# Performance work log

Measured on AMD Instinct MI355X. Metric: run time of the kernel, lower is better.

The kernel has to match this reference:

```python
import jax, jax.numpy as jnp
import numpy as np

N_NODES = 100000
N_EDGES = 1600000
IN_DIM = 64
HID_DIM = 64
OUT_DIM = 1


def setup_inputs() -> dict:
    key = jax.random.key(0)
    ks = jax.random.split(key, 5)
    x = jax.random.normal(ks[0], (N_NODES, IN_DIM), dtype=jnp.float32)
    edge_index = jax.random.randint(ks[1], (2, N_EDGES), 0, N_NODES, dtype=jnp.int64)
    s1 = 1.0 / np.sqrt(IN_DIM)
    s2 = 1.0 / np.sqrt(HID_DIM)
    W1 = jax.random.normal(ks[2], (IN_DIM, HID_DIM), dtype=jnp.float32) * s1
    b1 = jnp.zeros((HID_DIM,), dtype=jnp.float32)
    W2 = jax.random.normal(ks[3], (HID_DIM, HID_DIM), dtype=jnp.float32) * s2
    b2 = jnp.zeros((HID_DIM,), dtype=jnp.float32)
    Wp = jax.random.normal(ks[4], (HID_DIM, OUT_DIM), dtype=jnp.float32) * s2
    bp = jnp.zeros((OUT_DIM,), dtype=jnp.float32)
    return {"x": x, "edge_index": edge_index, "W1": W1, "b1": b1,
            "W2": W2, "b2": b2, "Wp": Wp, "bp": bp}


def _gcn_conv(x, src, dst, deg_inv_sqrt, W, b):
    # PyG GCNConv: linear transform, then deg-normalized scatter-add aggregation
    h = x @ W  # [N, out]
    norm = deg_inv_sqrt[src] * deg_inv_sqrt[dst]  # [E_total]
    msg = h[src] * norm[:, None]  # gather + scale, [E_total, out]
    agg = jax.ops.segment_sum(msg, dst, num_segments=x.shape[0])
    return agg + b


def reference(x, edge_index, W1, b1, W2, b2, Wp, bp):
    n = x.shape[0]
    # add self-loops (as PyG GCNConv does by default)
    loop = jnp.arange(n, dtype=edge_index.dtype)
    src = jnp.concatenate([edge_index[0], loop])
    dst = jnp.concatenate([edge_index[1], loop])
    # symmetric normalization from in-degree over dst (includes self-loops)
    deg = jax.ops.segment_sum(jnp.ones_like(dst, dtype=x.dtype), dst, num_segments=n)
    deg_inv_sqrt = jnp.where(deg > 0, jax.lax.rsqrt(jnp.maximum(deg, 1e-12)), 0.0)
    h = jax.nn.relu(_gcn_conv(x, src, dst, deg_inv_sqrt, W1, b1))
    # dropout(p=0.3) is identity at eval time
    h = jax.nn.relu(_gcn_conv(h, src, dst, deg_inv_sqrt, W2, b2))
    return h @ Wp + bp  # [N, OUT_DIM]
```

## Files before the change

### kernel.cpp

```cpp
#include <hip/hip_runtime.h>
#include <hip/hip_fp16.h>


#define GNN_N 100000
#define GNN_E 1600000
#define NBUCK 391
#define NBLK  250
#define EPB   6400
#define SCTILE 16
#define STAGE_CAP 4864
#define DUMMY_OFF (GNN_N * 128)

__global__ __launch_bounds__(256) void k_hist(const int* __restrict__ dst,
                                              int* __restrict__ hist,
                                              __half* __restrict__ TA,
                                              __half* __restrict__ TB) {
    __shared__ int h[NBUCK];
    for (int i = threadIdx.x; i < NBUCK; i += 256) h[i] = 0;
    if (blockIdx.x == 0 && threadIdx.x < 16) {
        uint4 z = {0, 0, 0, 0};
        int t = threadIdx.x;
        __half* base = (t < 8) ? TA : TB;
        *(uint4*)((char*)base + DUMMY_OFF + (t & 7) * 16) = z;
    }
    __syncthreads();
    int b = blockIdx.x;
    int e0 = b * EPB, e1 = min(e0 + EPB, GNN_E);
    for (int e = e0 + threadIdx.x * 4; e < e1; e += 1024) {
        int4 d = *(const int4*)(dst + e);
        atomicAdd(&h[d.x >> 8], 1);
        atomicAdd(&h[d.y >> 8], 1);
        atomicAdd(&h[d.z >> 8], 1);
        atomicAdd(&h[d.w >> 8], 1);
    }
    __syncthreads();
    for (int i = threadIdx.x; i < NBUCK; i += 256)
        hist[b * NBUCK + i] = h[i];
}

__global__ __launch_bounds__(256) void k_cscan(int* __restrict__ hist,
                                               int* __restrict__ tot) {
    __shared__ int tile[256][SCTILE + 1];
    int k0 = blockIdx.x * SCTILE;
    int b = threadIdx.x;
#pragma unroll
    for (int i = 0; i < SCTILE; ++i) {
        int k = k0 + i;
        tile[b][i] = (k < NBUCK && b < NBLK) ? hist[b * NBUCK + k] : 0;
    }
    __syncthreads();
    int lane = b & 63, w = b >> 6;
    int cSub = lane >> 4;
    int l16 = lane & 15;
    int col = w * 4 + cSub;
    int run = 0;
    for (int chunk = 0; chunk < 16; ++chunk) {
        int idx = chunk * 16 + l16;
        int v = tile[idx][col];
        int s = v;
#pragma unroll
        for (int o = 1; o < 16; o <<= 1) {
            int t = __shfl_up(s, o);
            if (l16 >= o) s += t;
        }
        tile[idx][col] = s - v + run;
        run += __shfl(s, lane | 15);
    }
    if (l16 == 0 && k0 + col < NBUCK) tot[k0 + col] = run;
    __syncthreads();
#pragma unroll
    for (int i = 0; i < SCTILE; ++i) {
        int k = k0 + i;
        if (k < NBUCK && b < NBLK) hist[b * NBUCK + k] = tile[b][i];
    }
}

__global__ __launch_bounds__(512) void k_btot(const int* __restrict__ tot,
                                              int* __restrict__ bbase,
                                              int* __restrict__ cbase) {
    __shared__ int s[NBUCK];
    int t = threadIdx.x;
    if (t < NBUCK) s[t] = tot[t];
    __syncthreads();
    if (t == 0) {
        int run = 0;
        for (int i = 0; i < NBUCK; ++i) { int v = s[i]; s[i] = run; run += v; }
    }
    __syncthreads();
    if (t < NBUCK) {
        bbase[t] = s[t];
        cbase[t] = (s[t] & ~3) + t * 772;
    }
    if (t == 0) bbase[NBUCK] = GNN_E;
}

__global__ __launch_bounds__(256) void k_part(const int* __restrict__ src,
                                              const int* __restrict__ dst,
                                              const int* __restrict__ hist,
                                              const int* __restrict__ bbase,
                                              unsigned int* __restrict__ part) {
    __shared__ int off[NBUCK];
    int b = blockIdx.x;
    for (int i = threadIdx.x; i < NBUCK; i += 256)
        off[i] = bbase[i] + hist[b * NBUCK + i];
    __syncthreads();
    int e0 = b * EPB, e1 = min(e0 + EPB, GNN_E);
    for (int e = e0 + threadIdx.x * 4; e < e1; e += 1024) {
        int4 d = *(const int4*)(dst + e);
        int4 s = *(const int4*)(src + e);
        int sl0 = atomicAdd(&off[d.x >> 8], 1);
        part[sl0] = ((unsigned int)(d.x & 255) << 17) | (unsigned int)s.x;
        int sl1 = atomicAdd(&off[d.y >> 8], 1);
        part[sl1] = ((unsigned int)(d.y & 255) << 17) | (unsigned int)s.y;
        int sl2 = atomicAdd(&off[d.z >> 8], 1);
        part[sl2] = ((unsigned int)(d.z & 255) << 17) | (unsigned int)s.z;
        int sl3 = atomicAdd(&off[d.w >> 8], 1);
        part[sl3] = ((unsigned int)(d.w & 255) << 17) | (unsigned int)s.w;
    }
}

__global__ __launch_bounds__(256) void k_bsort(const unsigned int* __restrict__ part,
                                               const int* __restrict__ bbase,
                                               const int* __restrict__ cbase,
                                               int* __restrict__ csr,
                                               int* __restrict__ rowptr,
                                               int* __restrict__ deg,
                                               float* __restrict__ dis) {
    __shared__ int cnt[256];
    __shared__ int pstart[256];
    __shared__ int bump[256];
    __shared__ unsigned int stage[STAGE_CAP];
    int k = blockIdx.x;
    int t = threadIdx.x;
    cnt[t] = 0;
    __syncthreads();
    int e0 = bbase[k], e1 = bbase[k + 1];
    int m = e1 - e0;
    bool fits = (m <= STAGE_CAP);
    for (int i = t; i < m; i += 256) {
        unsigned int p = part[e0 + i];
        if (fits) stage[i] = p;
        atomicAdd(&cnt[p >> 17], 1);
    }
    __syncthreads();
    if (t == 0) {
        int run = 0;
        for (int i = 0; i < 256; ++i) {
            pstart[i] = run;
            run += (cnt[i] + 3) & ~3;
        }
    }
    __syncthreads();
    int cb = cbase[k];
    int node = k * 256 + t;
    if (node < GNN_N) {
        int c = cnt[t];
        rowptr[node] = cb + pstart[t];
        deg[node]    = (c + 3) & ~3;
        dis[node]    = rsqrtf((float)c + 1.0f);
    }
    bump[t] = pstart[t];
    __syncthreads();
    for (int i = t; i < m; i += 256) {
        unsigned int p = fits ? stage[i] : part[e0 + i];
        int slot = atomicAdd(&bump[p >> 17], 1);
        csr[cb + slot] = (int)(p & 0x1FFFF) << 7;
    }
    __syncthreads();
    if (node < GNN_N) {
        int c = cnt[t], pc = (c + 3) & ~3;
        for (int i = c; i < pc; ++i)
            csr[cb + pstart[t] + i] = DUMMY_OFF;
    }
}

template<typename TIN>
__global__ __launch_bounds__(256) void k_mm64h(const TIN* __restrict__ X,
                                               const float* __restrict__ W,
                                               const float* __restrict__ dis,
                                               __half* __restrict__ Y, int n) {
    __shared__ float  Xs[64][68];
    __shared__ float4 Wsh[64 * 16];
    int tid = threadIdx.x;
    int base = blockIdx.x * 64;
    for (int i = tid; i < 1024; i += 256)
        Wsh[i] = ((const float4*)W)[i];
    if constexpr (sizeof(TIN) == 4) {
#pragma unroll
        for (int i = 0; i < 4; ++i) {
            int g = i * 256 + tid;
            int r = g >> 4, c4 = g & 15;
            int row = base + r;
            float4 v = (row < n) ? ((const float4*)(X + (size_t)row * 64))[c4]
                                 : make_float4(0.f, 0.f, 0.f, 0.f);
            *(float4*)&Xs[r][c4 * 4] = v;
        }
    } else {
#pragma unroll
        for (int i = 0; i < 2; ++i) {
            int g = i * 256 + tid;
            int r = g >> 3, c8 = g & 7;
            int row = base + r;
            float f[8];
            if (row < n) {
                uint4 u = *(const uint4*)((const __half*)X + (size_t)row * 64 + c8 * 8);
                float2 t0 = __half22float2(*(__half2*)&u.x);
                float2 t1 = __half22float2(*(__half2*)&u.y);
                float2 t2 = __half22float2(*(__half2*)&u.z);
                float2 t3 = __half22float2(*(__half2*)&u.w);
                f[0] = t0.x; f[1] = t0.y; f[2] = t1.x; f[3] = t1.y;
                f[4] = t2.x; f[5] = t2.y; f[6] = t3.x; f[7] = t3.y;
            } else {
#pragma unroll
                for (int z = 0; z < 8; ++z) f[z] = 0.f;
            }
            *(float4*)&Xs[r][c8 * 8 + 0] = make_float4(f[0], f[1], f[2], f[3]);
            *(float4*)&Xs[r][c8 * 8 + 4] = make_float4(f[4], f[5], f[6], f[7]);
        }
    }
    __syncthreads();
    int tj = tid & 15;
    int ti = tid >> 4;
    float4 a0 = {0,0,0,0}, a1 = {0,0,0,0}, a2 = {0,0,0,0}, a3 = {0,0,0,0};
#pragma unroll 1
    for (int k4 = 0; k4 < 16; ++k4) {
        float4 x0 = *(const float4*)&Xs[ti * 4 + 0][k4 * 4];
        float4 x1 = *(const float4*)&Xs[ti * 4 + 1][k4 * 4];
        float4 x2 = *(const float4*)&Xs[ti * 4 + 2][k4 * 4];
        float4 x3 = *(const float4*)&Xs[ti * 4 + 3][k4 * 4];
        float4 w0 = Wsh[(k4 * 4 + 0) * 16 + tj];
        float4 w1 = Wsh[(k4 * 4 + 1) * 16 + tj];
        float4 w2 = Wsh[(k4 * 4 + 2) * 16 + tj];
        float4 w3 = Wsh[(k4 * 4 + 3) * 16 + tj];
#define FMA4(A, XV)                                                      \
        A.x += XV.x * w0.x + XV.y * w1.x + XV.z * w2.x + XV.w * w3.x;    \
        A.y += XV.x * w0.y + XV.y * w1.y + XV.z * w2.y + XV.w * w3.y;    \
        A.z += XV.x * w0.z + XV.y * w1.z + XV.z * w2.z + XV.w * w3.z;    \
        A.w += XV.x * w0.w + XV.y * w1.w + XV.z * w2.w + XV.w * w3.w;
        FMA4(a0, x0) FMA4(a1, x1) FMA4(a2, x2) FMA4(a3, x3)
#undef FMA4
    }
#pragma unroll
    for (int q = 0; q < 4; ++q) {
        int row = base + ti * 4 + q;
        if (row < n) {
            float d = dis[row];
            float4 a = (q == 0) ? a0 : (q == 1) ? a1 : (q == 2) ? a2 : a3;
            __half2 p0 = __floats2half2_rn(a.x * d, a.y * d);
            __half2 p1 = __floats2half2_rn(a.z * d, a.w * d);
            __half2* yp = (__half2*)(Y + (size_t)row * 64);
            yp[tj * 2 + 0] = p0;
            yp[tj * 2 + 1] = p1;
        }
    }
}

#define ACC8(A, U) {                                                     \
    float2 f_;                                                           \
    f_ = __half22float2(*(__half2*)&U.x); A[0] += f_.x; A[1] += f_.y;    \
    f_ = __half22float2(*(__half2*)&U.y); A[2] += f_.x; A[3] += f_.y;    \
    f_ = __half22float2(*(__half2*)&U.z); A[4] += f_.x; A[5] += f_.y;    \
    f_ = __half22float2(*(__half2*)&U.w); A[6] += f_.x; A[7] += f_.y; }

template<bool HEAD>
__global__ __launch_bounds__(256) void k_gatherg(
        const __half* __restrict__ T, const int* __restrict__ csr,
        const int* __restrict__ rowptr, const int* __restrict__ deg,
        const float* __restrict__ dis, const float* __restrict__ bias,
        const float* __restrict__ Wp, const float* __restrict__ bp,
        void* __restrict__ outv, int n) {
    int tid = threadIdx.x;
    int q = tid & 7;
    int node = blockIdx.x * 32 + (tid >> 3);
    if (node >= n) return;
    int base = rowptr[node];
    int cnt  = deg[node];
    float dd = dis[node];
    const char* Tq = (const char*)T + q * 16;
    float a0[8], a1[8];
#pragma unroll
    for (int i = 0; i < 8; ++i) { a0[i] = 0.f; a1[i] = 0.f; }
    int j = 0;
    for (; j + 8 <= cnt; j += 8) {
        int4 c0 = *(const int4*)(csr + base + j);
        int4 c1 = *(const int4*)(csr + base + j + 4);
        uint4 u0 = *(const uint4*)(Tq + (size_t)(unsigned)c0.x);
        uint4 u1 = *(const uint4*)(Tq + (size_t)(unsigned)c0.y);
        uint4 u2 = *(const uint4*)(Tq + (size_t)(unsigned)c0.z);
        uint4 u3 = *(const uint4*)(Tq + (size_t)(unsigned)c0.w);
        uint4 u4 = *(const uint4*)(Tq + (size_t)(unsigned)c1.x);
        uint4 u5 = *(const uint4*)(Tq + (size_t)(unsigned)c1.y);
        uint4 u6 = *(const uint4*)(Tq + (size_t)(unsigned)c1.z);
        uint4 u7 = *(const uint4*)(Tq + (size_t)(unsigned)c1.w);
        ACC8(a0, u0) ACC8(a1, u1) ACC8(a0, u2) ACC8(a1, u3)
        ACC8(a0, u4) ACC8(a1, u5) ACC8(a0, u6) ACC8(a1, u7)
    }
    if (j < cnt) {
        int4 c0 = *(const int4*)(csr + base + j);
        uint4 u0 = *(const uint4*)(Tq + (size_t)(unsigned)c0.x);
        uint4 u1 = *(const uint4*)(Tq + (size_t)(unsigned)c0.y);
        uint4 u2 = *(const uint4*)(Tq + (size_t)(unsigned)c0.z);
        uint4 u3 = *(const uint4*)(Tq + (size_t)(unsigned)c0.w);
        ACC8(a0, u0) ACC8(a1, u1) ACC8(a0, u2) ACC8(a1, u3)
    }
    uint4 us = *(const uint4*)(Tq + (size_t)node * 128);
    ACC8(a1, us)
    float4 bb0 = ((const float4*)bias)[q * 2 + 0];
    float4 bb1 = ((const float4*)bias)[q * 2 + 1];
    float r[8];
    r[0] = fmaxf(dd * (a0[0] + a1[0]) + bb0.x, 0.f);
    r[1] = fmaxf(dd * (a0[1] + a1[1]) + bb0.y, 0.f);
    r[2] = fmaxf(dd * (a0[2] + a1[2]) + bb0.z, 0.f);
    r[3] = fmaxf(dd * (a0[3] + a1[3]) + bb0.w, 0.f);
    r[4] = fmaxf(dd * (a0[4] + a1[4]) + bb1.x, 0.f);
    r[5] = fmaxf(dd * (a0[5] + a1[5]) + bb1.y, 0.f);
    r[6] = fmaxf(dd * (a0[6] + a1[6]) + bb1.z, 0.f);
    r[7] = fmaxf(dd * (a0[7] + a1[7]) + bb1.w, 0.f);
    if constexpr (HEAD) {
        float4 w0 = ((const float4*)Wp)[q * 2 + 0];
        float4 w1 = ((const float4*)Wp)[q * 2 + 1];
        float s = r[0] * w0.x + r[1] * w0.y + r[2] * w0.z + r[3] * w0.w
                + r[4] * w1.x + r[5] * w1.y + r[6] * w1.z + r[7] * w1.w;
#pragma unroll
        for (int m = 1; m <= 4; m <<= 1) s += __shfl_xor(s, m);
        if (q == 0) ((float*)outv)[node] = s + bp[0];
    } else {
        __half* op = (__half*)outv + (size_t)node * 64 + q * 8;
        __half2 h0 = __floats2half2_rn(r[0], r[1]);
        __half2 h1 = __floats2half2_rn(r[2], r[3]);
        __half2 h2 = __floats2half2_rn(r[4], r[5]);
        __half2 h3 = __floats2half2_rn(r[6], r[7]);
        uint4 u;
        *(__half2*)&u.x = h0; *(__half2*)&u.y = h1;
        *(__half2*)&u.z = h2; *(__half2*)&u.w = h3;
        *(uint4*)op = u;
    }
}

extern "C" void kernel_launch(void* const* d_in, const int* in_sizes, int n_in,
                              void* d_out, int out_size, void* d_ws, size_t ws_size,
                              hipStream_t stream) {
    const float* x  = (const float*)d_in[0];
    const int*   ei = (const int*)d_in[1];
    const float* W1 = (const float*)d_in[2];
    const float* b1 = (const float*)d_in[3];
    const float* W2 = (const float*)d_in[4];
    const float* b2 = (const float*)d_in[5];
    const float* Wp = (const float*)d_in[6];
    const float* bp = (const float*)d_in[7];
    float* out = (float*)d_out;

    const int N = GNN_N, E = GNN_E;
    const int* srcv = ei;
    const int* dstv = ei + E;

    char* ws = (char*)d_ws;
    int*    hist   = (int*)(ws + 0);
    int*    bbase  = (int*)(ws + 392000);
    int*    cbase  = (int*)(ws + 393600);
    int*    rowptr = (int*)(ws + 395264);
    int*    deg    = (int*)(ws + 795264);
    float*  dis    = (float*)(ws + 1195264);
    int*    tot    = (int*)(ws + 1195264);
    int*    csr    = (int*)(ws + 1595392);
    __half* TA     = (__half*)(ws + 9600000);
    __half* h1h    = (__half*)(ws + 22400256);
    __half* TB     = (__half*)(ws + 35200384);
    unsigned int* part = (unsigned int*)(ws + 48000512);

    k_hist <<<NBLK, 256, 0, stream>>>(dstv, hist, TA, TB);
    k_cscan<<<(NBUCK + SCTILE - 1) / SCTILE, 256, 0, stream>>>(hist, tot);
    k_btot <<<1, 512, 0, stream>>>(tot, bbase, cbase);
    k_part <<<NBLK, 256, 0, stream>>>(srcv, dstv, hist, bbase, part);
    k_bsort<<<NBUCK, 256, 0, stream>>>(part, bbase, cbase, csr, rowptr, deg, dis);

    k_mm64h<float><<<(N + 63) / 64, 256, 0, stream>>>(x, W1, dis, TA, N);
    k_gatherg<false><<<(N + 31) / 32, 256, 0, stream>>>(TA, csr, rowptr, deg, dis,
                                                        b1, nullptr, nullptr, h1h, N);
    k_mm64h<__half><<<(N + 63) / 64, 256, 0, stream>>>(h1h, W2, dis, TB, N);
    k_gatherg<true><<<(N + 31) / 32, 256, 0, stream>>>(TB, csr, rowptr, deg, dis,
                                                       b2, Wp, bp, out, N);
}
```

Measured before the change: 147.7 us.

## Use MFMA for node transforms, parallelize scans, split histogram blocks

Replaces the FP32 FMA-based 64x64 node transform with fp16 MFMA 16x16x32 instructions, staging X and a transposed fp16 W in shared memory and writing the output through LDS for coalesced stores. Replaces the serial single-thread scans in k_btot and k_bsort with Hillis-Steele and wave-shuffle parallel scans. Doubles the number of histogram blocks, with k_cscan scanning in two passes and k_part reading the offset of every other sub-block. Inputs and weights are now rounded to fp16 before the matmul, which lowers precision, and k_part depends on its block aligning with an even histogram block.

New measurement: 132.0 us. -10.6%, faster.

```diff
diff --git a/kernel.cpp b/kernel.cpp
--- a/kernel.cpp
+++ b/kernel.cpp
@@ -5,11 +5,16 @@
 #define GNN_N 100000
 #define GNN_E 1600000
 #define NBUCK 391
+#define HBLK  500
+#define EPBH  3200
 #define NBLK  250
 #define EPB   6400
 #define SCTILE 16
 #define STAGE_CAP 4864
 #define DUMMY_OFF (GNN_N * 128)
+
+typedef _Float16 half8 __attribute__((ext_vector_type(8)));
+typedef float f32x4 __attribute__((ext_vector_type(4)));
 
 __global__ __launch_bounds__(256) void k_hist(const int* __restrict__ dst,
                                               int* __restrict__ hist,
@@ -25,7 +30,7 @@
     }
     __syncthreads();
     int b = blockIdx.x;
-    int e0 = b * EPB, e1 = min(e0 + EPB, GNN_E);
+    int e0 = b * EPBH, e1 = min(e0 + EPBH, GNN_E);
     for (int e = e0 + threadIdx.x * 4; e < e1; e += 1024) {
         int4 d = *(const int4*)(dst + e);
         atomicAdd(&h[d.x >> 8], 1);
@@ -43,53 +48,60 @@
     __shared__ int tile[256][SCTILE + 1];
     int k0 = blockIdx.x * SCTILE;
     int b = threadIdx.x;
-#pragma unroll
-    for (int i = 0; i < SCTILE; ++i) {
-        int k = k0 + i;
-        tile[b][i] = (k < NBUCK && b < NBLK) ? hist[b * NBUCK + k] : 0;
-    }
-    __syncthreads();
     int lane = b & 63, w = b >> 6;
     int cSub = lane >> 4;
     int l16 = lane & 15;
     int col = w * 4 + cSub;
     int run = 0;
-    for (int chunk = 0; chunk < 16; ++chunk) {
-        int idx = chunk * 16 + l16;
-        int v = tile[idx][col];
-        int s = v;
-#pragma unroll
-        for (int o = 1; o < 16; o <<= 1) {
-            int t = __shfl_up(s, o);
-            if (l16 >= o) s += t;
-        }
-        tile[idx][col] = s - v + run;
-        run += __shfl(s, lane | 15);
+    for (int pass = 0; pass < 2; ++pass) {
+        int r = pass * 256 + b;
+#pragma unroll
+        for (int i = 0; i < SCTILE; ++i) {
+            int k = k0 + i;
+            tile[b][i] = (k < NBUCK && r < HBLK) ? hist[r * NBUCK + k] : 0;
+        }
+        __syncthreads();
+        for (int chunk = 0; chunk < 16; ++chunk) {
+            int idx = chunk * 16 + l16;
+            int v = tile[idx][col];
+            int s = v;
+#pragma unroll
+            for (int o = 1; o < 16; o <<= 1) {
+                int t = __shfl_up(s, o);
+                if (l16 >= o) s += t;
+            }
+            tile[idx][col] = s - v + run;
+            run += __shfl(s, lane | 15);
+        }
+        __syncthreads();
+#pragma unroll
+        for (int i = 0; i < SCTILE; ++i) {
+            int k = k0 + i;
+            if (k < NBUCK && r < HBLK) hist[r * NBUCK + k] = tile[b][i];
+        }
+        __syncthreads();
     }
     if (l16 == 0 && k0 + col < NBUCK) tot[k0 + col] = run;
-    __syncthreads();
-#pragma unroll
-    for (int i = 0; i < SCTILE; ++i) {
-        int k = k0 + i;
-        if (k < NBUCK && b < NBLK) hist[b * NBUCK + k] = tile[b][i];
-    }
 }
 
 __global__ __launch_bounds__(512) void k_btot(const int* __restrict__ tot,
                                               int* __restrict__ bbase,
                                               int* __restrict__ cbase) {
-    __shared__ int s[NBUCK];
+    __shared__ int s[512];
     int t = threadIdx.x;
-    if (t < NBUCK) s[t] = tot[t];
-    __syncthreads();
-    if (t == 0) {
-        int run = 0;
-        for (int i = 0; i < NBUCK; ++i) { int v = s[i]; s[i] = run; run += v; }
-    }
-    __syncthreads();
+    int own = (t < NBUCK) ? tot[t] : 0;
+    s[t] = own;
+    __syncthreads();
+    for (int off = 1; off < 512; off <<= 1) {
+        int v = (t >= off) ? s[t - off] : 0;
+        __syncthreads();
+        s[t] += v;
+        __syncthreads();
+    }
     if (t < NBUCK) {
-        bbase[t] = s[t];
-        cbase[t] = (s[t] & ~3) + t * 772;
+        int ex = s[t] - own;
+        bbase[t] = ex;
+        cbase[t] = (ex & ~3) + t * 772;
     }
     if (t == 0) bbase[NBUCK] = GNN_E;
 }
@@ -102,7 +114,7 @@
     __shared__ int off[NBUCK];
     int b = blockIdx.x;
     for (int i = threadIdx.x; i < NBUCK; i += 256)
-        off[i] = bbase[i] + hist[b * NBUCK + i];
+        off[i] = bbase[i] + hist[(2 * b) * NBUCK + i];
     __syncthreads();
     int e0 = b * EPB, e1 = min(e0 + EPB, GNN_E);
     for (int e = e0 + threadIdx.x * 4; e < e1; e += 1024) {
@@ -129,6 +141,7 @@
     __shared__ int cnt[256];
     __shared__ int pstart[256];
     __shared__ int bump[256];
+    __shared__ int wtot[4];
     __shared__ unsigned int stage[STAGE_CAP];
     int k = blockIdx.x;
     int t = threadIdx.x;
@@ -143,24 +156,30 @@
         atomicAdd(&cnt[p >> 17], 1);
     }
     __syncthreads();
-    if (t == 0) {
-        int run = 0;
-        for (int i = 0; i < 256; ++i) {
-            pstart[i] = run;
-            run += (cnt[i] + 3) & ~3;
-        }
-    }
+    int c = cnt[t];
+    int padded = (c + 3) & ~3;
+    int v = padded;
+#pragma unroll
+    for (int o = 1; o < 64; o <<= 1) {
+        int u = __shfl_up(v, o);
+        if ((t & 63) >= o) v += u;
+    }
+    if ((t & 63) == 63) wtot[t >> 6] = v;
+    __syncthreads();
+    int wb = 0;
+#pragma unroll
+    for (int j = 0; j < 4; ++j)
+        if (j < (t >> 6)) wb += wtot[j];
+    pstart[t] = wb + v - padded;
+    bump[t] = pstart[t];
     __syncthreads();
     int cb = cbase[k];
     int node = k * 256 + t;
     if (node < GNN_N) {
-        int c = cnt[t];
         rowptr[node] = cb + pstart[t];
-        deg[node]    = (c + 3) & ~3;
+        deg[node]    = padded;
         dis[node]    = rsqrtf((float)c + 1.0f);
     }
-    bump[t] = pstart[t];
-    __syncthreads();
     for (int i = t; i < m; i += 256) {
         unsigned int p = fits ? stage[i] : part[e0 + i];
         int slot = atomicAdd(&bump[p >> 17], 1);
@@ -168,90 +187,80 @@
     }
     __syncthreads();
     if (node < GNN_N) {
-        int c = cnt[t], pc = (c + 3) & ~3;
-        for (int i = c; i < pc; ++i)
+        for (int i = c; i < padded; ++i)
             csr[cb + pstart[t] + i] = DUMMY_OFF;
     }
 }
 
 template<typename TIN>
-__global__ __launch_bounds__(256) void k_mm64h(const TIN* __restrict__ X,
-                                               const float* __restrict__ W,
-                                               const float* __restrict__ dis,
-                                               __half* __restrict__ Y, int n) {
-    __shared__ float  Xs[64][68];
-    __shared__ float4 Wsh[64 * 16];
+__global__ __launch_bounds__(256) void k_mmf(const TIN* __restrict__ X,
+                                             const float* __restrict__ W,
+                                             const float* __restrict__ dis,
+                                             __half* __restrict__ Y, int n) {
+    __shared__ __align__(16) __half Xs[64][72];
+    __shared__ __align__(16) __half Wt[64][72];
+    __shared__ float disS[64];
     int tid = threadIdx.x;
     int base = blockIdx.x * 64;
-    for (int i = tid; i < 1024; i += 256)
-        Wsh[i] = ((const float4*)W)[i];
+    for (int i = tid; i < 4096; i += 256) {
+        int k = i >> 6, j = i & 63;
+        Wt[j][k] = __float2half(W[i]);
+    }
+    if (tid < 64) disS[tid] = (base + tid < n) ? dis[base + tid] : 0.f;
     if constexpr (sizeof(TIN) == 4) {
 #pragma unroll
-        for (int i = 0; i < 4; ++i) {
-            int g = i * 256 + tid;
-            int r = g >> 4, c4 = g & 15;
+        for (int ii = 0; ii < 4; ++ii) {
+            int i = ii * 256 + tid;
+            int r = i >> 4, c4 = i & 15;
             int row = base + r;
-            float4 v = (row < n) ? ((const float4*)(X + (size_t)row * 64))[c4]
-                                 : make_float4(0.f, 0.f, 0.f, 0.f);
-            *(float4*)&Xs[r][c4 * 4] = v;
+            float4 vv = (row < n) ? ((const float4*)(X + (size_t)row * 64))[c4]
+                                  : make_float4(0.f, 0.f, 0.f, 0.f);
+            *(__half2*)&Xs[r][c4 * 4 + 0] = __floats2half2_rn(vv.x, vv.y);
+            *(__half2*)&Xs[r][c4 * 4 + 2] = __floats2half2_rn(vv.z, vv.w);
         }
     } else {
 #pragma unroll
-        for (int i = 0; i < 2; ++i) {
-            int g = i * 256 + tid;
-            int r = g >> 3, c8 = g & 7;
+        for (int ii = 0; ii < 2; ++ii) {
+            int i = ii * 256 + tid;
+            int r = i >> 3, c8 = i & 7;
             int row = base + r;
-            float f[8];
-            if (row < n) {
-                uint4 u = *(const uint4*)((const __half*)X + (size_t)row * 64 + c8 * 8);
-                float2 t0 = __half22float2(*(__half2*)&u.x);
-                float2 t1 = __half22float2(*(__half2*)&u.y);
-                float2 t2 = __half22float2(*(__half2*)&u.z);
-                float2 t3 = __half22float2(*(__half2*)&u.w);
-                f[0] = t0.x; f[1] = t0.y; f[2] = t1.x; f[3] = t1.y;
-                f[4] = t2.x; f[5] = t2.y; f[6] = t3.x; f[7] = t3.y;
-            } else {
-#pragma unroll
-                for (int z = 0; z < 8; ++z) f[z] = 0.f;
-            }
-            *(float4*)&Xs[r][c8 * 8 + 0] = make_float4(f[0], f[1], f[2], f[3]);
-            *(float4*)&Xs[r][c8 * 8 + 4] = make_float4(f[4], f[5], f[6], f[7]);
-        }
-    }
-    __syncthreads();
-    int tj = tid & 15;
-    int ti = tid >> 4;
-    float4 a0 = {0,0,0,0}, a1 = {0,0,0,0}, a2 = {0,0,0,0}, a3 = {0,0,0,0};
-#pragma unroll 1
-    for (int k4 = 0; k4 < 16; ++k4) {
-        float4 x0 = *(const float4*)&Xs[ti * 4 + 0][k4 * 4];
-        float4 x1 = *(const float4*)&Xs[ti * 4 + 1][k4 * 4];
-        float4 x2 = *(const float4*)&Xs[ti * 4 + 2][k4 * 4];
-        float4 x3 = *(const float4*)&Xs[ti * 4 + 3][k4 * 4];
-        float4 w0 = Wsh[(k4 * 4 + 0) * 16 + tj];
-        float4 w1 = Wsh[(k4 * 4 + 1) * 16 + tj];
-        float4 w2 = Wsh[(k4 * 4 + 2) * 16 + tj];
-        float4 w3 = Wsh[(k4 * 4 + 3) * 16 + tj];
-#define FMA4(A, XV)                                                      \
-        A.x += XV.x * w0.x + XV.y * w1.x + XV.z * w2.x + XV.w * w3.x;    \
-        A.y += XV.x * w0.y + XV.y * w1.y + XV.z * w2.y + XV.w * w3.y;    \
-        A.z += XV.x * w0.z + XV.y * w1.z + XV.z * w2.z + XV.w * w3.z;    \
-        A.w += XV.x * w0.w + XV.y * w1.w + XV.z * w2.w + XV.w * w3.w;
-        FMA4(a0, x0) FMA4(a1, x1) FMA4(a2, x2) FMA4(a3, x3)
-#undef FMA4
-    }
-#pragma unroll
-    for (int q = 0; q < 4; ++q) {
-        int row = base + ti * 4 + q;
-        if (row < n) {
-            float d = dis[row];
-            float4 a = (q == 0) ? a0 : (q == 1) ? a1 : (q == 2) ? a2 : a3;
-            __half2 p0 = __floats2half2_rn(a.x * d, a.y * d);
-            __half2 p1 = __floats2half2_rn(a.z * d, a.w * d);
-            __half2* yp = (__half2*)(Y + (size_t)row * 64);
-            yp[tj * 2 + 0] = p0;
-            yp[tj * 2 + 1] = p1;
-        }
+            uint4 u = {0, 0, 0, 0};
+            if (row < n)
+                u = *(const uint4*)((const __half*)X + (size_t)row * 64 + c8 * 8);
+            *(uint4*)&Xs[r][c8 * 8] = u;
+        }
+    }
+    __syncthreads();
+    int w = tid >> 6, lane = tid & 63;
+    int ar = w * 16 + (lane & 15);
+    int ak = (lane >> 4) * 8;
+    half8 a0 = *(const half8*)&Xs[ar][ak];
+    half8 a1 = *(const half8*)&Xs[ar][32 + ak];
+    f32x4 acc0 = {0.f, 0.f, 0.f, 0.f}, acc1 = acc0, acc2 = acc0, acc3 = acc0;
+#define MMCOL(ACC, C) {                                                   \
+        half8 b0 = *(const half8*)&Wt[(C) * 16 + (lane & 15)][ak];        \
+        half8 b1 = *(const half8*)&Wt[(C) * 16 + (lane & 15)][32 + ak];   \
+        ACC = __builtin_amdgcn_mfma_f32_16x16x32_f16(a0, b0, ACC, 0, 0, 0); \
+        ACC = __builtin_amdgcn_mfma_f32_16x16x32_f16(a1, b1, ACC, 0, 0, 0); }
+    MMCOL(acc0, 0) MMCOL(acc1, 1) MMCOL(acc2, 2) MMCOL(acc3, 3)
+#undef MMCOL
+    __syncthreads();
+#define DST(ACC, C) {                                                     \
+        _Pragma("unroll")                                                 \
+        for (int i = 0; i < 4; ++i) {                                     \
+            int rl = w * 16 + (lane >> 4) * 4 + i;                        \
+            Xs[rl][(C) * 16 + (lane & 15)] = __float2half(ACC[i] * disS[rl]); \
+        } }
+    DST(acc0, 0) DST(acc1, 1) DST(acc2, 2) DST(acc3, 3)
+#undef DST
+    __syncthreads();
+#pragma unroll
+    for (int ii = 0; ii < 2; ++ii) {
+        int i = ii * 256 + tid;
+        int r = i >> 3, c8 = i & 7;
+        int row = base + r;
+        if (row < n)
+            *(uint4*)(Y + (size_t)row * 64 + c8 * 8) = *(const uint4*)&Xs[r][c8 * 8];
     }
 }
 
@@ -326,13 +335,11 @@
         if (q == 0) ((float*)outv)[node] = s + bp[0];
     } else {
         __half* op = (__half*)outv + (size_t)node * 64 + q * 8;
-        __half2 h0 = __floats2half2_rn(r[0], r[1]);
-        __half2 h1 = __floats2half2_rn(r[2], r[3]);
-        __half2 h2 = __floats2half2_rn(r[4], r[5]);
-        __half2 h3 = __floats2half2_rn(r[6], r[7]);
         uint4 u;
-        *(__half2*)&u.x = h0; *(__half2*)&u.y = h1;
-        *(__half2*)&u.z = h2; *(__half2*)&u.w = h3;
+        *(__half2*)&u.x = __floats2half2_rn(r[0], r[1]);
+        *(__half2*)&u.y = __floats2half2_rn(r[2], r[3]);
+        *(__half2*)&u.z = __floats2half2_rn(r[4], r[5]);
+        *(__half2*)&u.w = __floats2half2_rn(r[6], r[7]);
         *(uint4*)op = u;
     }
 }
@@ -356,28 +363,28 @@
 
     char* ws = (char*)d_ws;
     int*    hist   = (int*)(ws + 0);
-    int*    bbase  = (int*)(ws + 392000);
-    int*    cbase  = (int*)(ws + 393600);
-    int*    rowptr = (int*)(ws + 395264);
-    int*    deg    = (int*)(ws + 795264);
-    float*  dis    = (float*)(ws + 1195264);
-    int*    tot    = (int*)(ws + 1195264);
-    int*    csr    = (int*)(ws + 1595392);
-    __half* TA     = (__half*)(ws + 9600000);
-    __half* h1h    = (__half*)(ws + 22400256);
-    __half* TB     = (__half*)(ws + 35200384);
-    unsigned int* part = (unsigned int*)(ws + 48000512);
-
-    k_hist <<<NBLK, 256, 0, stream>>>(dstv, hist, TA, TB);
+    int*    bbase  = (int*)(ws + 784000);
+    int*    cbase  = (int*)(ws + 785600);
+    int*    rowptr = (int*)(ws + 787200);
+    int*    deg    = (int*)(ws + 1187200);
+    float*  dis    = (float*)(ws + 1587200);
+    int*    tot    = (int*)(ws + 1587200);
+    int*    csr    = (int*)(ws + 1987200);
+    __half* TA     = (__half*)(ws + 9597440);
+    __half* h1h    = (__half*)(ws + 22410368);
+    __half* TB     = (__half*)(ws + 35210368);
+    unsigned int* part = (unsigned int*)(ws + 48023296);
+
+    k_hist <<<HBLK, 256, 0, stream>>>(dstv, hist, TA, TB);
     k_cscan<<<(NBUCK + SCTILE - 1) / SCTILE, 256, 0, stream>>>(hist, tot);
     k_btot <<<1, 512, 0, stream>>>(tot, bbase, cbase);
     k_part <<<NBLK, 256, 0, stream>>>(srcv, dstv, hist, bbase, part);
     k_bsort<<<NBUCK, 256, 0, stream>>>(part, bbase, cbase, csr, rowptr, deg, dis);
 
-    k_mm64h<float><<<(N + 63) / 64, 256, 0, stream>>>(x, W1, dis, TA, N);
+    k_mmf<float><<<(N + 63) / 64, 256, 0, stream>>>(x, W1, dis, TA, N);
     k_gatherg<false><<<(N + 31) / 32, 256, 0, stream>>>(TA, csr, rowptr, deg, dis,
                                                         b1, nullptr, nullptr, h1h, N);
-    k_mm64h<__half><<<(N + 63) / 64, 256, 0, stream>>>(h1h, W2, dis, TB, N);
+    k_mmf<__half><<<(N + 63) / 64, 256, 0, stream>>>(h1h, W2, dis, TB, N);
     k_gatherg<true><<<(N + 31) / 32, 256, 0, stream>>>(TB, csr, rowptr, deg, dis,
                                                        b2, Wp, bp, out, N);
 }
```
